# Performance work log

Measured on AMD Instinct MI355X. Metric: run time of the kernel, lower is better.

The kernel has to match this reference:

```python
import jax, jax.numpy as jnp
import numpy as np

DIM = 2048
STATE = 16
BATCH = 2
SEQ = 2048
LN_EPS = 1e-5


def setup_inputs() -> dict:
    key = jax.random.key(0)
    ks = jax.random.split(key, 12)
    d, n = DIM, STATE
    inp = {
        "x": jax.random.normal(ks[0], (BATCH, SEQ, d), dtype=jnp.float32),
        "ln_gamma": jnp.ones((d,), dtype=jnp.float32),
        "ln_beta": jnp.zeros((d,), dtype=jnp.float32),
        # proj_in: Linear(d, 2d) (spectral-normed; weights treated as effective)
        "W_in": jax.random.normal(ks[1], (2 * d, d), dtype=jnp.float32) / np.sqrt(d),
        "b_in": jnp.zeros((2 * d,), dtype=jnp.float32),
        "state_A": jax.random.normal(ks[2], (n, d), dtype=jnp.float32) * 0.01,
        "W_B": jax.random.normal(ks[3], (n, d), dtype=jnp.float32) / np.sqrt(d),
        "b_B": jnp.zeros((n,), dtype=jnp.float32),
        "W_C": jax.random.normal(ks[4], (n, d), dtype=jnp.float32) / np.sqrt(d),
        "b_C": jnp.zeros((n,), dtype=jnp.float32),
        "W_dt": jax.random.normal(ks[5], (d, d), dtype=jnp.float32) / np.sqrt(d),
        "b_dt": jnp.zeros((d,), dtype=jnp.float32),
        "W_out": jax.random.normal(ks[6], (d, d), dtype=jnp.float32) / np.sqrt(d),
        "b_out": jnp.zeros((d,), dtype=jnp.float32),
    }
    return inp


def reference(x, ln_gamma, ln_beta, W_in, b_in, state_A, W_B, b_B, W_C, b_C,
              W_dt, b_dt, W_out, b_out):
    residual = x
    # LayerNorm over last dim
    mu = jnp.mean(x, axis=-1, keepdims=True)
    var = jnp.mean(jnp.square(x - mu), axis=-1, keepdims=True)
    xn = (x - mu) * jax.lax.rsqrt(var + LN_EPS) * ln_gamma + ln_beta
    # input projection and gate split
    xz = jnp.einsum('bsd,ed->bse', xn, W_in) + b_in          # (B,S,2D)
    x_ssm, z = jnp.split(xz, 2, axis=-1)                      # (B,S,D) each
    # dt = clamp(softplus(proj_dt(x_ssm)), max=1.0)
    dt = jnp.minimum(jax.nn.softplus(jnp.einsum('bsd,ed->bse', x_ssm, W_dt) + b_dt), 1.0)
    Bm = jnp.einsum('bsd,nd->bsn', x_ssm, W_B) + b_B          # (B,S,N)
    Cm = jnp.einsum('bsd,nd->bsn', x_ssm, W_C) + b_C          # (B,S,N)
    # A_bar[b,s,n,d] = exp(state_A[n,d] * dt[b,s,d])
    A_bar = jnp.exp(state_A[None, None, :, :] * dt[:, :, None, :])  # (B,S,N,D)
    # y[b,s,d] = sum_n C[b,s,n]*B[b,s,n]*A_bar[b,s,n,d] * x_ssm[b,s,d]
    y = jnp.einsum('bsn,bsnd->bsd', Cm * Bm, A_bar) * x_ssm
    gated = y * jax.nn.silu(z)
    out = jnp.einsum('bsd,ed->bse', gated, W_out) + b_out
    return out + residual
```

## Files before the change

### kernel.cpp

```cpp
#include <hip/hip_runtime.h>

typedef unsigned short u16;
typedef float f32x4 __attribute__((ext_vector_type(4)));
typedef __bf16 bf16x8 __attribute__((ext_vector_type(8)));

__device__ __forceinline__ u16 f2bf(float f) {
    unsigned u = __float_as_uint(f);
    u += 0x7FFFu + ((u >> 16) & 1u);
    return (u16)(u >> 16);
}
__device__ __forceinline__ float b2f(u16 h) {
    return __uint_as_float(((unsigned)h) << 16);
}

__device__ __forceinline__ void async16(const u16* g, u16* l) {
    __builtin_amdgcn_global_load_lds(
        (__attribute__((address_space(1))) void*)(u16*)g,
        (__attribute__((address_space(3))) void*)l,
        16, 0, 0);
}

#define T_TOK 4096
#define DIM   2048

__global__ __launch_bounds__(256) void castw_kernel(const float* __restrict__ src,
                                                    u16* __restrict__ dst, int n4) {
    int i = blockIdx.x * 256 + threadIdx.x;
    if (i < n4) {
        float4 f = ((const float4*)src)[i];
        ushort4 u;
        u.x = f2bf(f.x); u.y = f2bf(f.y); u.z = f2bf(f.z); u.w = f2bf(f.w);
        ((ushort4*)dst)[i] = u;
    }
}

__global__ __launch_bounds__(256) void cast4_kernel(const float* __restrict__ s0, u16* __restrict__ d0, int n0,
                                                    const float* __restrict__ s1, u16* __restrict__ d1, int n1,
                                                    const float* __restrict__ s2, u16* __restrict__ d2, int n2,
                                                    const float* __restrict__ s3, u16* __restrict__ d3, int n3) {
    int j = blockIdx.x * 256 + threadIdx.x;
    const float* s; u16* d;
    if (j < n0) { s = s0; d = d0; }
    else {
        j -= n0;
        if (j < n1) { s = s1; d = d1; }
        else {
            j -= n1;
            if (j < n2) { s = s2; d = d2; }
            else { j -= n2; if (j >= n3) return; s = s3; d = d3; }
        }
    }
    float4 f = ((const float4*)s)[j];
    ushort4 u;
    u.x = f2bf(f.x); u.y = f2bf(f.y); u.z = f2bf(f.z); u.w = f2bf(f.w);
    ((ushort4*)d)[j] = u;
}

__global__ __launch_bounds__(256) void ln_cast_kernel(const float* __restrict__ x,
                                                      const float* __restrict__ g,
                                                      const float* __restrict__ b,
                                                      u16* __restrict__ o) {
    __shared__ float s1[4], s2[4];
    int t = blockIdx.x, tid = threadIdx.x;
    int wave = tid >> 6, lane = tid & 63;
    size_t base = (size_t)t * DIM;
    int d0 = tid * 8;
    float4 v0 = *(const float4*)(x + base + d0);
    float4 v1 = *(const float4*)(x + base + d0 + 4);
    float v[8] = {v0.x, v0.y, v0.z, v0.w, v1.x, v1.y, v1.z, v1.w};
    float s = 0.f;
#pragma unroll
    for (int j = 0; j < 8; ++j) s += v[j];
#pragma unroll
    for (int o2 = 32; o2; o2 >>= 1) s += __shfl_xor(s, o2);
    if (lane == 0) s1[wave] = s;
    __syncthreads();
    float mu = (s1[0] + s1[1] + s1[2] + s1[3]) * (1.f / DIM);
    float q = 0.f;
#pragma unroll
    for (int j = 0; j < 8; ++j) { float dd = v[j] - mu; q += dd * dd; }
#pragma unroll
    for (int o2 = 32; o2; o2 >>= 1) q += __shfl_xor(q, o2);
    if (lane == 0) s2[wave] = q;
    __syncthreads();
    float var = (s2[0] + s2[1] + s2[2] + s2[3]) * (1.f / DIM);
    float rs = rsqrtf(var + 1e-5f);
    float4 g0 = *(const float4*)(g + d0), g1 = *(const float4*)(g + d0 + 4);
    float4 b0 = *(const float4*)(b + d0), b1 = *(const float4*)(b + d0 + 4);
    float gv[8] = {g0.x, g0.y, g0.z, g0.w, g1.x, g1.y, g1.z, g1.w};
    float bv[8] = {b0.x, b0.y, b0.z, b0.w, b1.x, b1.y, b1.z, b1.w};
    ushort4 r0, r1;
    u16* rp0 = (u16*)&r0; u16* rp1 = (u16*)&r1;
#pragma unroll
    for (int j = 0; j < 4; ++j) {
        rp0[j] = f2bf((v[j] - mu) * rs * gv[j] + bv[j]);
        rp1[j] = f2bf((v[j + 4] - mu) * rs * gv[j + 4] + bv[j + 4]);
    }
    *(ushort4*)(o + base + d0) = r0;
    *(ushort4*)(o + base + d0 + 4) = r1;
}

#define BM 128
#define BN 128
#define BK 32

__global__ __launch_bounds__(256) void gemm_wide(const u16* __restrict__ A, int lda,
                                                 const u16* __restrict__ W, int ldw,
                                                 const float* __restrict__ bias,
                                                 u16* __restrict__ Xs,
                                                 u16* __restrict__ Z, int K) {
    __shared__ __align__(16) u16 lAB[2 * BM * BK];
    const int tid = threadIdx.x;
    const int wave = tid >> 6, lane = tid & 63;
    const int quad = lane >> 4, l16 = lane & 15;
    const int tM = blockIdx.x * BM;
    const int tN = blockIdx.y * BN;
    const int wr = wave >> 1, wc = wave & 1;

    const bool isB = (wave >= 2);
    const u16* src = isB ? W : A;
    const int srcld = isB ? ldw : lda;
    const int rowbase = (isB ? tN : tM) + (wave & 1) * 64 + (lane >> 2);
    const int colofs = (lane & 3) * 8;
    const u16* gptr[4];
    u16* ldst[4];
#pragma unroll
    for (int i = 0; i < 4; ++i) {
        gptr[i] = src + (size_t)(rowbase + i * 16) * srcld + colofs;
        ldst[i] = &lAB[(wave * 4 + i) * 512];
    }

    const u16* lA = lAB;
    const u16* lB = lAB + BM * BK;
    int a_off[4], b_off[4];
#pragma unroll
    for (int i = 0; i < 4; ++i) {
        a_off[i] = (wr * 64 + i * 16 + l16) * BK + quad * 8;
        b_off[i] = (wc * 64 + i * 16 + l16) * BK + quad * 8;
    }

    f32x4 acc[4][4] = {};

    for (int kt = 0; kt < K; kt += BK) {
#pragma unroll
        for (int i = 0; i < 4; ++i) async16(gptr[i] + kt, ldst[i]);
        __syncthreads();
        bf16x8 af[4], bfr[4];
#pragma unroll
        for (int i = 0; i < 4; ++i) af[i] = *(const bf16x8*)&lA[a_off[i]];
#pragma unroll
        for (int i = 0; i < 4; ++i) bfr[i] = *(const bf16x8*)&lB[b_off[i]];
#pragma unroll
        for (int mi = 0; mi < 4; ++mi)
#pragma unroll
            for (int ni = 0; ni < 4; ++ni)
                acc[mi][ni] = __builtin_amdgcn_mfma_f32_16x16x32_bf16(
                    af[mi], bfr[ni], acc[mi][ni], 0, 0, 0);
        __syncthreads();
    }

    const bool isb_z = (tN >= 2048);
    u16* dst = isb_z ? Z : Xs;
#pragma unroll
    for (int mi = 0; mi < 4; ++mi) {
#pragma unroll
        for (int ni = 0; ni < 4; ++ni) {
            int col = tN + wc * 64 + ni * 16 + l16;
            float bv = bias[col];
            int ocol = isb_z ? (col - 2048) : col;
#pragma unroll
            for (int r = 0; r < 4; ++r) {
                int row = tM + wr * 64 + mi * 16 + quad * 4 + r;
                dst[(size_t)row * 2048 + ocol] = f2bf(acc[mi][ni][r] + bv);
            }
        }
    }
}

#define NBM 128
#define NBN 64
#define NBK 64

template <int EPI>
__global__ __launch_bounds__(256) void gemm_nw(const u16* __restrict__ A, int lda,
                                               const u16* __restrict__ W, int ldw,
                                               const float* __restrict__ bias,
                                               const float* __restrict__ resid,
                                               void* __restrict__ C, int ldc, int K,
                                               u16* __restrict__ dots) {
    __shared__ __align__(16) u16 lAB[(NBM + NBN) * NBK];
    const int tid = threadIdx.x;
    const int wave = tid >> 6, lane = tid & 63;
    const int quad = lane >> 4, l16 = lane & 15;
    const int tM = blockIdx.x * NBM;
    const int tN = blockIdx.y * NBN;
    const int wr = wave >> 1, wc = wave & 1;

    const int rowin = tid >> 3;
    const int r3 = rowin & 7;
    const int col8 = ((tid & 7) ^ r3) * 8;
    const u16* gptr[6];
    u16* ldst[6];
#pragma unroll
    for (int i = 0; i < 6; ++i) {
        int trow = i * 32 + rowin;
        const u16* src = (i < 4) ? (A + (size_t)(tM + trow) * lda)
                                 : (W + (size_t)(tN + (trow - NBM)) * ldw);
        gptr[i] = src + col8;
        ldst[i] = &lAB[(i * 32 + wave * 8) * NBK];
    }

    int a_off[2][4], b_off[2][2];
#pragma unroll
    for (int h = 0; h < 2; ++h) {
#pragma unroll
        for (int mi = 0; mi < 4; ++mi)
            a_off[h][mi] = (wr * 64 + mi * 16 + l16) * NBK +
                           (((h * 4 + quad) ^ (l16 & 7)) * 8);
#pragma unroll
        for (int ni = 0; ni < 2; ++ni)
            b_off[h][ni] = (NBM + wc * 32 + ni * 16 + l16) * NBK +
                           (((h * 4 + quad) ^ (l16 & 7)) * 8);
    }

    f32x4 acc[4][2] = {};

    for (int kt = 0; kt < K; kt += NBK) {
#pragma unroll
        for (int i = 0; i < 6; ++i) async16(gptr[i] + kt, ldst[i]);
        __syncthreads();
        bf16x8 af[2][4], bfr[2][2];
#pragma unroll
        for (int h = 0; h < 2; ++h) {
#pragma unroll
            for (int mi = 0; mi < 4; ++mi) af[h][mi] = *(const bf16x8*)&lAB[a_off[h][mi]];
#pragma unroll
            for (int ni = 0; ni < 2; ++ni) bfr[h][ni] = *(const bf16x8*)&lAB[b_off[h][ni]];
        }
#pragma unroll
        for (int h = 0; h < 2; ++h)
#pragma unroll
            for (int mi = 0; mi < 4; ++mi)
#pragma unroll
                for (int ni = 0; ni < 2; ++ni)
                    acc[mi][ni] = __builtin_amdgcn_mfma_f32_16x16x32_bf16(
                        af[h][mi], bfr[h][ni], acc[mi][ni], 0, 0, 0);
        __syncthreads();
    }

#pragma unroll
    for (int mi = 0; mi < 4; ++mi) {
#pragma unroll
        for (int ni = 0; ni < 2; ++ni) {
            int col = tN + wc * 32 + ni * 16 + l16;
            float bv = (EPI == 1 && col >= 2048) ? 0.f : bias[col];
#pragma unroll
            for (int r = 0; r < 4; ++r) {
                int row = tM + wr * 64 + mi * 16 + quad * 4 + r;
                float v = acc[mi][ni][r] + bv;
                if constexpr (EPI == 1) {
                    if (col < 2048) {
                        float sp = (v > 20.f) ? v : log1pf(__expf(v));
                        ((u16*)C)[(size_t)row * ldc + col] = f2bf(fminf(sp, 1.0f));
                    } else if (col < 2080) {
                        dots[(size_t)row * 32 + (col - 2048)] = f2bf(v);
                    }
                } else {
                    size_t idx = (size_t)row * ldc + col;
                    ((float*)C)[idx] = v + resid[idx];
                }
            }
        }
    }
}

__global__ __launch_bounds__(256) void ssm_gate_kernel(const u16* __restrict__ dtb,
                                                       const u16* __restrict__ xsb,
                                                       const u16* __restrict__ zb,
                                                       const float* __restrict__ A,
                                                       const u16* __restrict__ dots,
                                                       const float* __restrict__ bB,
                                                       const float* __restrict__ bC,
                                                       u16* __restrict__ gated) {
    __shared__ float Pl[16];
    int t = blockIdx.x, tid = threadIdx.x;
    if (tid < 16) {
        float Bv = b2f(dots[(size_t)t * 32 + tid]) + bB[tid];
        float Cv = b2f(dots[(size_t)t * 32 + 16 + tid]) + bC[tid];
        Pl[tid] = Bv * Cv;
    }
    __syncthreads();
    size_t dbase = (size_t)t * DIM;
    int d0 = tid * 8;
    ushort4 dth[2], xsh[2], zh[2];
    dth[0] = *(const ushort4*)(dtb + dbase + d0);
    dth[1] = *(const ushort4*)(dtb + dbase + d0 + 4);
    xsh[0] = *(const ushort4*)(xsb + dbase + d0);
    xsh[1] = *(const ushort4*)(xsb + dbase + d0 + 4);
    zh[0]  = *(const ushort4*)(zb + dbase + d0);
    zh[1]  = *(const ushort4*)(zb + dbase + d0 + 4);
    float dtv[8], xsv[8], zv[8];
#pragma unroll
    for (int h = 0; h < 2; ++h) {
        const u16* dp = (const u16*)&dth[h];
        const u16* xp = (const u16*)&xsh[h];
        const u16* zp = (const u16*)&zh[h];
#pragma unroll
        for (int j = 0; j < 4; ++j) {
            dtv[h * 4 + j] = b2f(dp[j]);
            xsv[h * 4 + j] = b2f(xp[j]);
            zv[h * 4 + j]  = b2f(zp[j]);
        }
    }
    float s[8] = {};
#pragma unroll
    for (int n = 0; n < 16; ++n) {
        float4 a0 = *(const float4*)(A + n * DIM + d0);
        float4 a1 = *(const float4*)(A + n * DIM + d0 + 4);
        float pn = Pl[n];
        float av[8] = {a0.x, a0.y, a0.z, a0.w, a1.x, a1.y, a1.z, a1.w};
#pragma unroll
        for (int j = 0; j < 8; ++j) s[j] += pn * __expf(av[j] * dtv[j]);
    }
    ushort4 r0, r1;
    u16* rp0 = (u16*)&r0; u16* rp1 = (u16*)&r1;
#pragma unroll
    for (int j = 0; j < 8; ++j) {
        float y = s[j] * xsv[j];
        float sz = zv[j] * (1.0f / (1.0f + __expf(-zv[j])));
        u16 hv = f2bf(y * sz);
        if (j < 4) rp0[j] = hv; else rp1[j - 4] = hv;
    }
    *(ushort4*)(gated + dbase + d0) = r0;
    *(ushort4*)(gated + dbase + d0 + 4) = r1;
}

extern "C" void kernel_launch(void* const* d_in, const int* in_sizes, int n_in,
                              void* d_out, int out_size, void* d_ws, size_t ws_size,
                              hipStream_t stream) {
    const float* x      = (const float*)d_in[0];
    const float* ln_g   = (const float*)d_in[1];
    const float* ln_b   = (const float*)d_in[2];
    const float* W_in   = (const float*)d_in[3];
    const float* b_in   = (const float*)d_in[4];
    const float* stateA = (const float*)d_in[5];
    const float* W_B    = (const float*)d_in[6];
    const float* b_B    = (const float*)d_in[7];
    const float* W_C    = (const float*)d_in[8];
    const float* b_C    = (const float*)d_in[9];
    const float* W_dt   = (const float*)d_in[10];
    const float* b_dt   = (const float*)d_in[11];
    const float* W_out  = (const float*)d_in[12];
    const float* b_out  = (const float*)d_in[13];

    char* ws = (char*)d_ws;
    u16*   wb_in  = (u16*)(ws);
    u16*   wb_out = (u16*)(ws);
    u16*   xnb    = (u16*)(ws + 16777216);
    u16*   wb_dt  = (u16*)(ws + 16777216);
    u16*   gated  = (u16*)(ws + 16777216);
    u16*   xsb    = (u16*)(ws + 33554432);
    u16*   zb     = (u16*)(ws + 50331648);
    u16*   dtb    = (u16*)(ws + 67108864);
    u16*   dotsb  = (u16*)(ws + 83886080);

    castw_kernel<<<8192, 256, 0, stream>>>(W_in, wb_in, 2097152);
    ln_cast_kernel<<<T_TOK, 256, 0, stream>>>(x, ln_g, ln_b, xnb);
    gemm_wide<<<dim3(32, 32), 256, 0, stream>>>(xnb, 2048, wb_in, 2048, b_in,
                                                xsb, zb, 2048);
    cast4_kernel<<<8256, 256, 0, stream>>>(
        W_dt, wb_dt, 1048576,
        W_B,  wb_dt + (size_t)2048 * 2048, 8192,
        W_C,  wb_dt + (size_t)2064 * 2048, 8192,
        W_out, wb_out, 1048576);
    gemm_nw<1><<<dim3(32, 33), 256, 0, stream>>>(xsb, 2048, wb_dt, 2048, b_dt,
                                                 nullptr, dtb, 2048, 2048, dotsb);
    ssm_gate_kernel<<<T_TOK, 256, 0, stream>>>(dtb, xsb, zb, stateA, dotsb,
                                               b_B, b_C, gated);
    gemm_nw<2><<<dim3(32, 32), 256, 0, stream>>>(gated, 2048, wb_out, 2048, b_out,
                                                 x, (float*)d_out, 2048, 2048, nullptr);
}
```

Baseline: 434.8 us.

## Merge weight cast with layernorm and widen input GEMM K-tile with swizzled LDS

```diff
diff --git a/kernel.cpp b/kernel.cpp
--- a/kernel.cpp
+++ b/kernel.cpp
@@ -23,15 +23,59 @@
 #define T_TOK 4096
 #define DIM   2048
 
-__global__ __launch_bounds__(256) void castw_kernel(const float* __restrict__ src,
-                                                    u16* __restrict__ dst, int n4) {
-    int i = blockIdx.x * 256 + threadIdx.x;
-    if (i < n4) {
-        float4 f = ((const float4*)src)[i];
+__global__ __launch_bounds__(256) void castln_kernel(const float* __restrict__ W_in,
+                                                     u16* __restrict__ wb_in,
+                                                     const float* __restrict__ x,
+                                                     const float* __restrict__ g,
+                                                     const float* __restrict__ b,
+                                                     u16* __restrict__ o) {
+    __shared__ float s1[4], s2[4];
+    int blk = blockIdx.x, tid = threadIdx.x;
+    if (blk < 8192) {
+        int i = blk * 256 + tid;
+        float4 f = ((const float4*)W_in)[i];
         ushort4 u;
         u.x = f2bf(f.x); u.y = f2bf(f.y); u.z = f2bf(f.z); u.w = f2bf(f.w);
-        ((ushort4*)dst)[i] = u;
-    }
+        ((ushort4*)wb_in)[i] = u;
+        return;
+    }
+    int t = blk - 8192;
+    int wave = tid >> 6, lane = tid & 63;
+    size_t base = (size_t)t * DIM;
+    int d0 = tid * 8;
+    float4 v0 = *(const float4*)(x + base + d0);
+    float4 v1 = *(const float4*)(x + base + d0 + 4);
+    float v[8] = {v0.x, v0.y, v0.z, v0.w, v1.x, v1.y, v1.z, v1.w};
+    float s = 0.f;
+#pragma unroll
+    for (int j = 0; j < 8; ++j) s += v[j];
+#pragma unroll
+    for (int o2 = 32; o2; o2 >>= 1) s += __shfl_xor(s, o2);
+    if (lane == 0) s1[wave] = s;
+    __syncthreads();
+    float mu = (s1[0] + s1[1] + s1[2] + s1[3]) * (1.f / DIM);
+    float q = 0.f;
+#pragma unroll
+    for (int j = 0; j < 8; ++j) { float dd = v[j] - mu; q += dd * dd; }
+#pragma unroll
+    for (int o2 = 32; o2; o2 >>= 1) q += __shfl_xor(q, o2);
+    if (lane == 0) s2[wave] = q;
+    __syncthreads();
+    float var = (s2[0] + s2[1] + s2[2] + s2[3]) * (1.f / DIM);
+    float rs = rsqrtf(var + 1e-5f);
+    float4 g0 = *(const float4*)(g + d0), g1 = *(const float4*)(g + d0 + 4);
+    float4 b0 = *(const float4*)(b + d0), b1 = *(const float4*)(b + d0 + 4);
+    float gv[8] = {g0.x, g0.y, g0.z, g0.w, g1.x, g1.y, g1.z, g1.w};
+    float bv[8] = {b0.x, b0.y, b0.z, b0.w, b1.x, b1.y, b1.z, b1.w};
+    ushort4 r0, r1;
+    u16* rp0 = (u16*)&r0; u16* rp1 = (u16*)&r1;
+#pragma unroll
+    for (int j = 0; j < 4; ++j) {
+        rp0[j] = f2bf((v[j] - mu) * rs * gv[j] + bv[j]);
+        rp1[j] = f2bf((v[j + 4] - mu) * rs * gv[j + 4] + bv[j + 4]);
+    }
+    *(ushort4*)(o + base + d0) = r0;
+    *(ushort4*)(o + base + d0 + 4) = r1;
 }
 
 __global__ __launch_bounds__(256) void cast4_kernel(const float* __restrict__ s0, u16* __restrict__ d0, int n0,
@@ -56,106 +100,69 @@
     ((ushort4*)d)[j] = u;
 }
 
-__global__ __launch_bounds__(256) void ln_cast_kernel(const float* __restrict__ x,
-                                                      const float* __restrict__ g,
-                                                      const float* __restrict__ b,
-                                                      u16* __restrict__ o) {
-    __shared__ float s1[4], s2[4];
-    int t = blockIdx.x, tid = threadIdx.x;
-    int wave = tid >> 6, lane = tid & 63;
-    size_t base = (size_t)t * DIM;
-    int d0 = tid * 8;
-    float4 v0 = *(const float4*)(x + base + d0);
-    float4 v1 = *(const float4*)(x + base + d0 + 4);
-    float v[8] = {v0.x, v0.y, v0.z, v0.w, v1.x, v1.y, v1.z, v1.w};
-    float s = 0.f;
-#pragma unroll
-    for (int j = 0; j < 8; ++j) s += v[j];
-#pragma unroll
-    for (int o2 = 32; o2; o2 >>= 1) s += __shfl_xor(s, o2);
-    if (lane == 0) s1[wave] = s;
-    __syncthreads();
-    float mu = (s1[0] + s1[1] + s1[2] + s1[3]) * (1.f / DIM);
-    float q = 0.f;
-#pragma unroll
-    for (int j = 0; j < 8; ++j) { float dd = v[j] - mu; q += dd * dd; }
-#pragma unroll
-    for (int o2 = 32; o2; o2 >>= 1) q += __shfl_xor(q, o2);
-    if (lane == 0) s2[wave] = q;
-    __syncthreads();
-    float var = (s2[0] + s2[1] + s2[2] + s2[3]) * (1.f / DIM);
-    float rs = rsqrtf(var + 1e-5f);
-    float4 g0 = *(const float4*)(g + d0), g1 = *(const float4*)(g + d0 + 4);
-    float4 b0 = *(const float4*)(b + d0), b1 = *(const float4*)(b + d0 + 4);
-    float gv[8] = {g0.x, g0.y, g0.z, g0.w, g1.x, g1.y, g1.z, g1.w};
-    float bv[8] = {b0.x, b0.y, b0.z, b0.w, b1.x, b1.y, b1.z, b1.w};
-    ushort4 r0, r1;
-    u16* rp0 = (u16*)&r0; u16* rp1 = (u16*)&r1;
-#pragma unroll
-    for (int j = 0; j < 4; ++j) {
-        rp0[j] = f2bf((v[j] - mu) * rs * gv[j] + bv[j]);
-        rp1[j] = f2bf((v[j + 4] - mu) * rs * gv[j + 4] + bv[j + 4]);
-    }
-    *(ushort4*)(o + base + d0) = r0;
-    *(ushort4*)(o + base + d0 + 4) = r1;
-}
-
-#define BM 128
-#define BN 128
-#define BK 32
-
-__global__ __launch_bounds__(256) void gemm_wide(const u16* __restrict__ A, int lda,
-                                                 const u16* __restrict__ W, int ldw,
+#define WBM 128
+#define WBN 128
+#define WBK 64
+
+__global__ __launch_bounds__(256) void gemm_wide(const u16* __restrict__ A,
+                                                 const u16* __restrict__ W,
                                                  const float* __restrict__ bias,
                                                  u16* __restrict__ Xs,
                                                  u16* __restrict__ Z, int K) {
-    __shared__ __align__(16) u16 lAB[2 * BM * BK];
+    __shared__ __align__(16) u16 lAB[(WBM + WBN) * WBK];
     const int tid = threadIdx.x;
     const int wave = tid >> 6, lane = tid & 63;
     const int quad = lane >> 4, l16 = lane & 15;
-    const int tM = blockIdx.x * BM;
-    const int tN = blockIdx.y * BN;
+    const int tM = blockIdx.x * WBM;
+    const int tN = blockIdx.y * WBN;
     const int wr = wave >> 1, wc = wave & 1;
 
-    const bool isB = (wave >= 2);
-    const u16* src = isB ? W : A;
-    const int srcld = isB ? ldw : lda;
-    const int rowbase = (isB ? tN : tM) + (wave & 1) * 64 + (lane >> 2);
-    const int colofs = (lane & 3) * 8;
-    const u16* gptr[4];
-    u16* ldst[4];
-#pragma unroll
-    for (int i = 0; i < 4; ++i) {
-        gptr[i] = src + (size_t)(rowbase + i * 16) * srcld + colofs;
-        ldst[i] = &lAB[(wave * 4 + i) * 512];
-    }
-
-    const u16* lA = lAB;
-    const u16* lB = lAB + BM * BK;
-    int a_off[4], b_off[4];
-#pragma unroll
-    for (int i = 0; i < 4; ++i) {
-        a_off[i] = (wr * 64 + i * 16 + l16) * BK + quad * 8;
-        b_off[i] = (wc * 64 + i * 16 + l16) * BK + quad * 8;
+    const int rowin = tid >> 3;
+    const int col8 = ((tid & 7) ^ (rowin & 7)) * 8;
+    const u16* gptr[8];
+    u16* ldst[8];
+#pragma unroll
+    for (int i = 0; i < 8; ++i) {
+        int trow = i * 32 + rowin;
+        const u16* src = (i < 4) ? (A + (size_t)(tM + trow) * 2048)
+                                 : (W + (size_t)(tN + (trow - WBM)) * 2048);
+        gptr[i] = src + col8;
+        ldst[i] = &lAB[(i * 32 + wave * 8) * WBK];
+    }
+
+    int a_off[2][4], b_off[2][4];
+#pragma unroll
+    for (int h = 0; h < 2; ++h) {
+#pragma unroll
+        for (int mi = 0; mi < 4; ++mi)
+            a_off[h][mi] = (wr * 64 + mi * 16 + l16) * WBK +
+                           (((h * 4 + quad) ^ (l16 & 7)) * 8);
+#pragma unroll
+        for (int ni = 0; ni < 4; ++ni)
+            b_off[h][ni] = (WBM + wc * 64 + ni * 16 + l16) * WBK +
+                           (((h * 4 + quad) ^ (l16 & 7)) * 8);
     }
 
     f32x4 acc[4][4] = {};
 
-    for (int kt = 0; kt < K; kt += BK) {
-#pragma unroll
-        for (int i = 0; i < 4; ++i) async16(gptr[i] + kt, ldst[i]);
+    for (int kt = 0; kt < K; kt += WBK) {
+#pragma unroll
+        for (int i = 0; i < 8; ++i) async16(gptr[i] + kt, ldst[i]);
         __syncthreads();
-        bf16x8 af[4], bfr[4];
-#pragma unroll
-        for (int i = 0; i < 4; ++i) af[i] = *(const bf16x8*)&lA[a_off[i]];
-#pragma unroll
-        for (int i = 0; i < 4; ++i) bfr[i] = *(const bf16x8*)&lB[b_off[i]];
-#pragma unroll
-        for (int mi = 0; mi < 4; ++mi)
-#pragma unroll
-            for (int ni = 0; ni < 4; ++ni)
-                acc[mi][ni] = __builtin_amdgcn_mfma_f32_16x16x32_bf16(
-                    af[mi], bfr[ni], acc[mi][ni], 0, 0, 0);
+#pragma unroll
+        for (int h = 0; h < 2; ++h) {
+            bf16x8 af[4], bfr[4];
+#pragma unroll
+            for (int i = 0; i < 4; ++i) af[i] = *(const bf16x8*)&lAB[a_off[h][i]];
+#pragma unroll
+            for (int i = 0; i < 4; ++i) bfr[i] = *(const bf16x8*)&lAB[b_off[h][i]];
+#pragma unroll
+            for (int mi = 0; mi < 4; ++mi)
+#pragma unroll
+                for (int ni = 0; ni < 4; ++ni)
+                    acc[mi][ni] = __builtin_amdgcn_mfma_f32_16x16x32_bf16(
+                        af[mi], bfr[ni], acc[mi][ni], 0, 0, 0);
+        }
         __syncthreads();
     }
 
@@ -364,10 +371,8 @@
     u16*   dtb    = (u16*)(ws + 67108864);
     u16*   dotsb  = (u16*)(ws + 83886080);
 
-    castw_kernel<<<8192, 256, 0, stream>>>(W_in, wb_in, 2097152);
-    ln_cast_kernel<<<T_TOK, 256, 0, stream>>>(x, ln_g, ln_b, xnb);
-    gemm_wide<<<dim3(32, 32), 256, 0, stream>>>(xnb, 2048, wb_in, 2048, b_in,
-                                                xsb, zb, 2048);
+    castln_kernel<<<12288, 256, 0, stream>>>(W_in, wb_in, x, ln_g, ln_b, xnb);
+    gemm_wide<<<dim3(32, 32), 256, 0, stream>>>(xnb, wb_in, b_in, xsb, zb, 2048);
     cast4_kernel<<<8256, 256, 0, stream>>>(
         W_dt, wb_dt, 1048576,
         W_B,  wb_dt + (size_t)2048 * 2048, 8192,
```

Measured after the change: 394.9 us. 9.2% less time.
